# Performance work log

Measured on AMD Instinct MI355X. Metric: run time of the kernel, lower is better.

Reference implementation:

```python
import jax, jax.numpy as jnp
import numpy as np

N_NODES = 100000
N_EDGES = 1600000
NFEAT = 128
NHID = 128
NCLASS = 40


def gcn_conv(x, W, b, src, dst, n_nodes):
    """PyG-style GCNConv: x' = D^{-1/2}(A+I)D^{-1/2} (x W) + b."""
    h = x @ W  # [N, out]
    loop = jnp.arange(n_nodes, dtype=src.dtype)
    s = jnp.concatenate([src, loop])  # add self-loops
    d = jnp.concatenate([dst, loop])
    deg = jax.ops.segment_sum(jnp.ones_like(s, dtype=h.dtype), d, num_segments=n_nodes)
    dinv = jnp.where(deg > 0, jax.lax.rsqrt(deg), 0.0)
    norm = dinv[s] * dinv[d]  # [E+N]
    msg = h[s] * norm[:, None]  # gather + scale
    out = jax.ops.segment_sum(msg, d, num_segments=n_nodes)  # scatter-add
    return out + b


def setup_inputs() -> dict:
    key = jax.random.key(0)
    ks = jax.random.split(key, 6)
    x = jax.random.normal(ks[0], (N_NODES, NFEAT), dtype=jnp.float32)
    edge_index = jax.random.randint(ks[1], (2, N_EDGES), 0, N_NODES, dtype=jnp.int64)
    sc1 = 1.0 / np.sqrt(NFEAT)
    sc2 = 1.0 / np.sqrt(NHID)
    W1 = jax.random.normal(ks[2], (NFEAT, NHID), dtype=jnp.float32) * sc1
    b1 = jnp.zeros((NHID,), dtype=jnp.float32)
    Wm = jax.random.normal(ks[3], (NHID, NHID), dtype=jnp.float32) * sc2
    bm = jnp.zeros((NHID,), dtype=jnp.float32)
    W2 = jax.random.normal(ks[4], (NHID, NCLASS), dtype=jnp.float32) * sc2
    b2 = jnp.zeros((NCLASS,), dtype=jnp.float32)
    return {"x": x, "edge_index": edge_index, "W1": W1, "b1": b1,
            "Wm": Wm, "bm": bm, "W2": W2, "b2": b2}


def reference(x, edge_index, W1, b1, Wm, bm, W2, b2):
    # StandGCNX forward, eval mode (dropout = identity)
    src, dst = edge_index[0], edge_index[1]
    n = x.shape[0]
    h = jax.nn.relu(gcn_conv(x, W1, b1, src, dst, n))
    h = jax.nn.relu(gcn_conv(h, Wm, bm, src, dst, n))
    out = gcn_conv(h, W2, b2, src, dst, n)
    return out
```

## Files before the change

### kernel.cpp

```cpp
#include <hip/hip_runtime.h>
#include <hip/hip_bf16.h>

typedef __attribute__((ext_vector_type(8))) short bf16x8;
typedef __attribute__((ext_vector_type(4))) float f32x4;

__device__ __forceinline__ ushort bf16rne(float f) {
    uint u = __float_as_uint(f);
    return (ushort)((u + 0x7fffu + ((u >> 16) & 1u)) >> 16);
}
__device__ __forceinline__ void unpack2(uint p, float& a, float& b) {
    a = __uint_as_float(p << 16);
    b = __uint_as_float(p & 0xffff0000u);
}


__global__ __launch_bounds__(256) void k_pre1(const float* __restrict__ W1,
                                              const float* __restrict__ Wm,
                                              const float* __restrict__ W2,
                                              ushort* __restrict__ w1t,
                                              ushort* __restrict__ wmt,
                                              ushort* __restrict__ w2t,
                                              const int* __restrict__ dst,
                                              int* __restrict__ bcnt, int E) {
    __shared__ int hist[512];
    int b = blockIdx.x;
    int t = threadIdx.x;
    if (b < 152) {
        if (b < 64) {
            int i = b * 256 + t; int k = i >> 7, n = i & 127;
            w1t[n * 128 + k] = bf16rne(W1[k * 128 + n]);
        } else if (b < 128) {
            int i = (b - 64) * 256 + t; int k = i >> 7, n = i & 127;
            wmt[n * 128 + k] = bf16rne(Wm[k * 128 + n]);
        } else {
            int i = (b - 128) * 256 + t;
            if (i < 6144) {
                int n = i >> 7, k = i & 127;
                w2t[n * 128 + k] = (n < 40) ? bf16rne(W2[k * 40 + n]) : (ushort)0;
            }
        }
        return;
    }
    hist[t] = 0; hist[t + 256] = 0;
    __syncthreads();
    int off = (b - 152) * 4096;
    int cnt = min(4096, E - off);
    for (int i = t; i < cnt; i += 256) atomicAdd(&hist[dst[off + i] >> 8], 1);
    __syncthreads();
    if (hist[t]) atomicAdd(&bcnt[t], hist[t]);
    if (hist[t + 256]) atomicAdd(&bcnt[t + 256], hist[t + 256]);
}

__global__ void k_bscan(const int* __restrict__ bcnt, int* __restrict__ bbase,
                        int* __restrict__ bcur, int nbuck) {
    __shared__ int s[512];
    int t = threadIdx.x;
    s[t] = (t < nbuck) ? bcnt[t] : 0;
    __syncthreads();
    for (int d = 1; d < 512; d <<= 1) {
        int u = (t >= d) ? s[t - d] : 0;
        __syncthreads();
        if (t >= d) s[t] += u;
        __syncthreads();
    }
    int excl = (t == 0) ? 0 : s[t - 1];
    bbase[t] = excl;
    if (t < nbuck) bcur[t] = excl;
    if (t == 511) bbase[512] = s[511];
}


__global__ __launch_bounds__(256) void k_pack_gemm(const int* __restrict__ src,
                                                   const int* __restrict__ dst,
                                                   int* __restrict__ bcur,
                                                   uint* __restrict__ pairbuf,
                                                   int E, int nbuck, int ntile,
                                                   const float* __restrict__ A,
                                                   const ushort* __restrict__ Wt,
                                                   ushort* __restrict__ C, int M) {
    __shared__ int hist[512];
    __shared__ int scn[512];
    __shared__ int cur[512];
    __shared__ int gbase[512];
    __shared__ uint sorted[4096];
    int t = threadIdx.x;
    if ((int)blockIdx.x >= ntile) {
        int blk = blockIdx.x - ntile;
        int wave = t >> 6, lane = t & 63;
        int m16 = lane & 15, quad = lane >> 4;
        int rowA = blk * 64 + wave * 16 + m16;
        int rA = min(rowA, M - 1);
        const float4* A4 = (const float4*)A;

        f32x4 acc[8];
#pragma unroll
        for (int i = 0; i < 8; i++) acc[i] = (f32x4){0.f, 0.f, 0.f, 0.f};
#pragma unroll
        for (int it = 0; it < 4; it++) {
            float4 f0 = A4[(size_t)rA * 32 + 8 * it + 2 * quad];
            float4 f1 = A4[(size_t)rA * 32 + 8 * it + 2 * quad + 1];
            bf16x8 af;
            af[0] = (short)bf16rne(f0.x); af[1] = (short)bf16rne(f0.y);
            af[2] = (short)bf16rne(f0.z); af[3] = (short)bf16rne(f0.w);
            af[4] = (short)bf16rne(f1.x); af[5] = (short)bf16rne(f1.y);
            af[6] = (short)bf16rne(f1.z); af[7] = (short)bf16rne(f1.w);
#pragma unroll
            for (int nt = 0; nt < 8; nt++) {
                bf16x8 bfr = *(const bf16x8*)(Wt + (size_t)(nt * 16 + m16) * 128 + it * 32 + quad * 8);
                acc[nt] = __builtin_amdgcn_mfma_f32_16x16x32_bf16(af, bfr, acc[nt], 0, 0, 0);
            }
        }
        int rowBase = blk * 64 + wave * 16 + quad * 4;
#pragma unroll
        for (int nt = 0; nt < 8; nt++) {
            int col = nt * 16 + m16;
#pragma unroll
            for (int r = 0; r < 4; r++) {
                int row = rowBase + r;
                if (row < M) C[(size_t)row * 128 + col] = bf16rne(acc[nt][r]);
            }
        }
        return;
    }
    int off = blockIdx.x * 4096;
    int cnt = min(4096, E - off);
    hist[t] = 0; hist[t + 256] = 0;
    __syncthreads();
    for (int i = t; i < cnt; i += 256) {
        int b = dst[off + i] >> 8;
        atomicAdd(&hist[b], 1);
    }
    __syncthreads();
    scn[t] = hist[t]; scn[t + 256] = hist[t + 256];
    __syncthreads();
    for (int d = 1; d < 256; d <<= 1) {
        int u0 = (t >= d) ? scn[t - d] : 0;
        int u1 = (t >= d) ? scn[256 + t - d] : 0;
        __syncthreads();
        if (t >= d) { scn[t] += u0; scn[256 + t] += u1; }
        __syncthreads();
    }
    int tot0 = scn[255];
    scn[256 + t] += tot0;
    __syncthreads();
    cur[t] = (t == 0) ? 0 : scn[t - 1];
    cur[t + 256] = scn[t + 255];
    if (t < nbuck && hist[t] > 0) gbase[t] = atomicAdd(&bcur[t], hist[t]);
    int t2 = t + 256;
    if (t2 < nbuck && hist[t2] > 0) gbase[t2] = atomicAdd(&bcur[t2], hist[t2]);
    __syncthreads();
    for (int i = t; i < cnt; i += 256) {
        int d = dst[off + i];
        int s = src[off + i];
        int b = d >> 8;
        int pos = atomicAdd(&cur[b], 1);
        sorted[pos] = ((uint)(d & 255) << 24) | (uint)s;
    }
    __syncthreads();
    int wid = t >> 6, lane = t & 63;
    for (int b = wid; b < nbuck; b += 4) {
        int n = hist[b];
        if (n == 0) continue;
        int ls = (b == 0) ? 0 : scn[b - 1];
        int gb = gbase[b];
        for (int j = lane; j < n; j += 64)
            pairbuf[gb + j] = sorted[ls + j];
    }
}

#define CSR_CAP 5632
__global__ __launch_bounds__(256) void k_csrbuild(const uint* __restrict__ pairbuf,
                                                  const int* __restrict__ bbase,
                                                  int* __restrict__ rowptr,
                                                  float* __restrict__ dinv,
                                                  int* __restrict__ csr,
                                                  int N, int nbuck) {
    __shared__ int lhist[256];
    __shared__ int scn[256];
    __shared__ int lcur[256];
    __shared__ int lcsr[CSR_CAP];
    int b = blockIdx.x;
    int base = b << 8;
    int nn = min(256, N - base);
    int lo = bbase[b], hi = bbase[b + 1];
    int cnt = hi - lo;
    int t = threadIdx.x;
    lhist[t] = 0;
    __syncthreads();
    for (int i = t; i < cnt; i += 256) atomicAdd(&lhist[pairbuf[lo + i] >> 24], 1);
    __syncthreads();
    int mydeg = lhist[t];
    scn[t] = mydeg;
    __syncthreads();
    for (int d = 1; d < 256; d <<= 1) {
        int u = (t >= d) ? scn[t - d] : 0;
        __syncthreads();
        if (t >= d) scn[t] += u;
        __syncthreads();
    }
    int excl = (t == 0) ? 0 : scn[t - 1];
    lcur[t] = excl;
    if (t < nn) {
        rowptr[base + t] = lo + excl;
        dinv[base + t] = rsqrtf((float)(mydeg + 1));
    }
    if (b == nbuck - 1 && t == 0) rowptr[N] = hi;
    __syncthreads();
    if (cnt <= CSR_CAP) {
        for (int i = t; i < cnt; i += 256) {
            uint p = pairbuf[lo + i];
            int pos = atomicAdd(&lcur[p >> 24], 1);
            lcsr[pos] = (int)(p & 0xFFFFFFu);
        }
        __syncthreads();
        for (int i = t; i < cnt; i += 256) csr[lo + i] = lcsr[i];
    } else {
        for (int i = t; i < cnt; i += 256) {
            uint p = pairbuf[lo + i];
            int pos = lo + atomicAdd(&lcur[p >> 24], 1);
            csr[pos] = (int)(p & 0xFFFFFFu);
        }
    }
}


template <int NT, bool EDGE_W>
__device__ __forceinline__ void fused_agg_gemm(const ushort* __restrict__ g,
                                               const float* __restrict__ dinv,
                                               const int* __restrict__ rowptr,
                                               const int* __restrict__ csr,
                                               const float* __restrict__ bias,
                                               const ushort* __restrict__ Wt,
                                               ushort* __restrict__ C,
                                               int M, int ccols) {
    __shared__ ushort hs[32][136];
    __shared__ int nextNode;
    int t = threadIdx.x;
    if (t == 0) nextNode = 0;
    int l = t & 15;
    const uint4* g16 = (const uint4*)g;
    float4 bb0 = ((const float4*)bias)[2 * l];
    float4 bb1 = ((const float4*)bias)[2 * l + 1];
    __syncthreads();

    for (;;) {
        int idx = 0;
        if (l == 0) idx = atomicAdd(&nextNode, 1);
        idx = __shfl(idx, (t & 63) & ~15, 64);
        if (idx >= 32) break;
        int node = blockIdx.x * 32 + idx;
        int nd = min(node, M - 1);
        float dn = dinv[nd];
        float a[8];
        {
            uint4 p = g16[(size_t)nd * 16 + l];
            float u, v;
            if (EDGE_W) {
                unpack2(p.x, u, v); a[0] = u * dn; a[1] = v * dn;
                unpack2(p.y, u, v); a[2] = u * dn; a[3] = v * dn;
                unpack2(p.z, u, v); a[4] = u * dn; a[5] = v * dn;
                unpack2(p.w, u, v); a[6] = u * dn; a[7] = v * dn;
            } else {
                unpack2(p.x, a[0], a[1]); unpack2(p.y, a[2], a[3]);
                unpack2(p.z, a[4], a[5]); unpack2(p.w, a[6], a[7]);
            }
        }
        int e0 = rowptr[nd], e1 = rowptr[nd + 1];
        int e = e0;
        for (; e + 4 <= e1; e += 4) {
            int s0 = csr[e], s1 = csr[e + 1], s2 = csr[e + 2], s3 = csr[e + 3];
            float w0 = 1.f, w1 = 1.f, w2 = 1.f, w3 = 1.f;
            if (EDGE_W) { w0 = dinv[s0]; w1 = dinv[s1]; w2 = dinv[s2]; w3 = dinv[s3]; }
            uint4 p0 = g16[(size_t)s0 * 16 + l];
            uint4 p1 = g16[(size_t)s1 * 16 + l];
            uint4 p2 = g16[(size_t)s2 * 16 + l];
            uint4 p3 = g16[(size_t)s3 * 16 + l];
            float u, v;
            if (EDGE_W) {
                unpack2(p0.x, u, v); a[0] += u * w0; a[1] += v * w0;
                unpack2(p0.y, u, v); a[2] += u * w0; a[3] += v * w0;
                unpack2(p0.z, u, v); a[4] += u * w0; a[5] += v * w0;
                unpack2(p0.w, u, v); a[6] += u * w0; a[7] += v * w0;
                unpack2(p1.x, u, v); a[0] += u * w1; a[1] += v * w1;
                unpack2(p1.y, u, v); a[2] += u * w1; a[3] += v * w1;
                unpack2(p1.z, u, v); a[4] += u * w1; a[5] += v * w1;
                unpack2(p1.w, u, v); a[6] += u * w1; a[7] += v * w1;
                unpack2(p2.x, u, v); a[0] += u * w2; a[1] += v * w2;
                unpack2(p2.y, u, v); a[2] += u * w2; a[3] += v * w2;
                unpack2(p2.z, u, v); a[4] += u * w2; a[5] += v * w2;
                unpack2(p2.w, u, v); a[6] += u * w2; a[7] += v * w2;
                unpack2(p3.x, u, v); a[0] += u * w3; a[1] += v * w3;
                unpack2(p3.y, u, v); a[2] += u * w3; a[3] += v * w3;
                unpack2(p3.z, u, v); a[4] += u * w3; a[5] += v * w3;
                unpack2(p3.w, u, v); a[6] += u * w3; a[7] += v * w3;
            } else {
                unpack2(p0.x, u, v); a[0] += u; a[1] += v;
                unpack2(p0.y, u, v); a[2] += u; a[3] += v;
                unpack2(p0.z, u, v); a[4] += u; a[5] += v;
                unpack2(p0.w, u, v); a[6] += u; a[7] += v;
                unpack2(p1.x, u, v); a[0] += u; a[1] += v;
                unpack2(p1.y, u, v); a[2] += u; a[3] += v;
                unpack2(p1.z, u, v); a[4] += u; a[5] += v;
                unpack2(p1.w, u, v); a[6] += u; a[7] += v;
                unpack2(p2.x, u, v); a[0] += u; a[1] += v;
                unpack2(p2.y, u, v); a[2] += u; a[3] += v;
                unpack2(p2.z, u, v); a[4] += u; a[5] += v;
                unpack2(p2.w, u, v); a[6] += u; a[7] += v;
                unpack2(p3.x, u, v); a[0] += u; a[1] += v;
                unpack2(p3.y, u, v); a[2] += u; a[3] += v;
                unpack2(p3.z, u, v); a[4] += u; a[5] += v;
                unpack2(p3.w, u, v); a[6] += u; a[7] += v;
            }
        }
        for (; e < e1; e++) {
            int s = csr[e];
            float w = EDGE_W ? dinv[s] : 1.f;
            uint4 p = g16[(size_t)s * 16 + l];
            float u, v;
            unpack2(p.x, u, v); a[0] += u * w; a[1] += v * w;
            unpack2(p.y, u, v); a[2] += u * w; a[3] += v * w;
            unpack2(p.z, u, v); a[4] += u * w; a[5] += v * w;
            unpack2(p.w, u, v); a[6] += u * w; a[7] += v * w;
        }
        float o0 = fmaxf(a[0] * dn + bb0.x, 0.f);
        float o1 = fmaxf(a[1] * dn + bb0.y, 0.f);
        float o2 = fmaxf(a[2] * dn + bb0.z, 0.f);
        float o3 = fmaxf(a[3] * dn + bb0.w, 0.f);
        float o4 = fmaxf(a[4] * dn + bb1.x, 0.f);
        float o5 = fmaxf(a[5] * dn + bb1.y, 0.f);
        float o6 = fmaxf(a[6] * dn + bb1.z, 0.f);
        float o7 = fmaxf(a[7] * dn + bb1.w, 0.f);
        uint4 qv;
        qv.x = (uint)bf16rne(o0) | ((uint)bf16rne(o1) << 16);
        qv.y = (uint)bf16rne(o2) | ((uint)bf16rne(o3) << 16);
        qv.z = (uint)bf16rne(o4) | ((uint)bf16rne(o5) << 16);
        qv.w = (uint)bf16rne(o6) | ((uint)bf16rne(o7) << 16);
        *(uint4*)&hs[idx][l * 8] = qv;
    }
    __syncthreads();

    int wave = t >> 6, lane = t & 63;
    int m16 = lane & 15, quad = lane >> 4;
    int rowHalf = wave & 1;
    int ntHalf = wave >> 1;
    constexpr int NTH = (NT + 1) / 2;
    int ntStart = ntHalf * NTH;
    int ntEnd = ntHalf ? NT : NTH;

    f32x4 acc[NTH];
#pragma unroll
    for (int i = 0; i < NTH; i++) acc[i] = (f32x4){0.f, 0.f, 0.f, 0.f};
#pragma unroll
    for (int it = 0; it < 4; it++) {
        bf16x8 af = *(const bf16x8*)&hs[rowHalf * 16 + m16][it * 32 + quad * 8];
        for (int nt = ntStart; nt < ntEnd; nt++) {
            bf16x8 bfr = *(const bf16x8*)(Wt + (size_t)(nt * 16 + m16) * 128 + it * 32 + quad * 8);
            acc[nt - ntStart] = __builtin_amdgcn_mfma_f32_16x16x32_bf16(af, bfr, acc[nt - ntStart], 0, 0, 0);
        }
    }
    int rowBase = blockIdx.x * 32 + rowHalf * 16 + quad * 4;
    float dnv[4];
#pragma unroll
    for (int r = 0; r < 4; r++) dnv[r] = dinv[min(rowBase + r, M - 1)];
    for (int nt = ntStart; nt < ntEnd; nt++) {
        int col = nt * 16 + m16;
        if (col >= ccols) continue;
#pragma unroll
        for (int r = 0; r < 4; r++) {
            int row = rowBase + r;
            if (row < M) C[(size_t)row * ccols + col] = bf16rne(acc[nt - ntStart][r] * dnv[r]);
        }
    }
}

__global__ __launch_bounds__(256) void k_fusedA(const ushort* __restrict__ g,
                                                const float* __restrict__ dinv,
                                                const int* __restrict__ rowptr,
                                                const int* __restrict__ csr,
                                                const float* __restrict__ bias,
                                                const ushort* __restrict__ Wt,
                                                ushort* __restrict__ C, int M) {
    fused_agg_gemm<8, true>(g, dinv, rowptr, csr, bias, Wt, C, M, 128);
}

__global__ __launch_bounds__(256) void k_fusedB(const ushort* __restrict__ g,
                                                const float* __restrict__ dinv,
                                                const int* __restrict__ rowptr,
                                                const int* __restrict__ csr,
                                                const float* __restrict__ bias,
                                                const ushort* __restrict__ Wt,
                                                ushort* __restrict__ C, int M) {
    fused_agg_gemm<3, false>(g, dinv, rowptr, csr, bias, Wt, C, M, 40);
}


__global__ __launch_bounds__(256) void k_agg40_b(const ushort* __restrict__ g3,
                                                 const float* __restrict__ dinv,
                                                 const int* __restrict__ rowptr,
                                                 const int* __restrict__ csr,
                                                 const float* __restrict__ bias,
                                                 float* __restrict__ out, int N) {
    int t = threadIdx.x;
    if (t >= 250) return;
    int grp = t / 10;
    int l = t - grp * 10;
    int node = blockIdx.x * 25 + grp;
    if (node >= N) return;
    const uint2* gp = (const uint2*)g3;
    float dn = dinv[node];
    float a0, a1, a2, a3;
    {
        uint2 p = gp[(size_t)node * 10 + l];
        unpack2(p.x, a0, a1);
        unpack2(p.y, a2, a3);
    }
    int e0 = rowptr[node], e1 = rowptr[node + 1];
    int e = e0;
    for (; e + 4 <= e1; e += 4) {
        int s0 = csr[e], s1 = csr[e + 1], s2 = csr[e + 2], s3 = csr[e + 3];
        uint2 p0 = gp[(size_t)s0 * 10 + l];
        uint2 p1 = gp[(size_t)s1 * 10 + l];
        uint2 p2 = gp[(size_t)s2 * 10 + l];
        uint2 p3 = gp[(size_t)s3 * 10 + l];
        float u, v;
        unpack2(p0.x, u, v); a0 += u; a1 += v;
        unpack2(p0.y, u, v); a2 += u; a3 += v;
        unpack2(p1.x, u, v); a0 += u; a1 += v;
        unpack2(p1.y, u, v); a2 += u; a3 += v;
        unpack2(p2.x, u, v); a0 += u; a1 += v;
        unpack2(p2.y, u, v); a2 += u; a3 += v;
        unpack2(p3.x, u, v); a0 += u; a1 += v;
        unpack2(p3.y, u, v); a2 += u; a3 += v;
    }
    for (; e < e1; e++) {
        int s = csr[e];
        uint2 p = gp[(size_t)s * 10 + l];
        float u, v;
        unpack2(p.x, u, v); a0 += u; a1 += v;
        unpack2(p.y, u, v); a2 += u; a3 += v;
    }
    float4 bb = ((const float4*)bias)[l];
    float4 o;
    o.x = a0 * dn + bb.x;
    o.y = a1 * dn + bb.y;
    o.z = a2 * dn + bb.z;
    o.w = a3 * dn + bb.w;
    ((float4*)out)[(size_t)node * 10 + l] = o;
}


extern "C" void kernel_launch(void* const* d_in, const int* in_sizes, int n_in,
                              void* d_out, int out_size, void* d_ws, size_t ws_size,
                              hipStream_t stream) {
    const float* x  = (const float*)d_in[0];
    const int* eidx = (const int*)d_in[1];
    const float* W1 = (const float*)d_in[2];
    const float* b1 = (const float*)d_in[3];
    const float* Wm = (const float*)d_in[4];
    const float* bm = (const float*)d_in[5];
    const float* W2 = (const float*)d_in[6];
    const float* b2 = (const float*)d_in[7];
    float* out = (float*)d_out;

    int N = in_sizes[0] / 128;
    int E = in_sizes[1] / 2;
    const int* src = eidx;
    const int* dst = eidx + E;
    int nbuck = (N + 255) >> 8;
    int ntile = (E + 4095) / 4096;

    char* ws = (char*)d_ws;
    size_t off = 0;
    auto alloc = [&](size_t bytes) -> void* {
        void* p = ws + off;
        off += (bytes + 255) & ~(size_t)255;
        return p;
    };
    float*  dinv    = (float*)alloc((size_t)N * 4);
    int*    rowptr  = (int*)alloc(((size_t)N + 1) * 4);
    int*    csr     = (int*)alloc((size_t)E * 4);
    uint*   pairbuf = (uint*)alloc((size_t)E * 4);
    int*    bcnt    = (int*)alloc(512 * 4);
    int*    bbase   = (int*)alloc(513 * 4);
    int*    bcur    = (int*)alloc(512 * 4);
    ushort* w1t     = (ushort*)alloc(128 * 128 * 2);
    ushort* wmt     = (ushort*)alloc(128 * 128 * 2);
    ushort* w2t     = (ushort*)alloc(48 * 128 * 2);
    ushort* gbuf    = (ushort*)alloc((size_t)N * 128 * 2);
    ushort* gbuf2   = (ushort*)alloc((size_t)N * 128 * 2);
    ushort* g3      = (ushort*)alloc((size_t)N * 40 * 2);

    int gblk64 = (N + 63) / 64;
    int gblk32 = (N + 31) / 32;

    hipMemsetAsync(bcnt, 0, 512 * 4, stream);
    k_pre1<<<152 + ntile, 256, 0, stream>>>(W1, Wm, W2, w1t, wmt, w2t, dst, bcnt, E);
    k_bscan<<<1, 512, 0, stream>>>(bcnt, bbase, bcur, nbuck);
    k_pack_gemm<<<ntile + gblk64, 256, 0, stream>>>(src, dst, bcur, pairbuf, E, nbuck,
                                                    ntile, x, w1t, gbuf, N);
    k_csrbuild<<<nbuck, 256, 0, stream>>>(pairbuf, bbase, rowptr, dinv, csr, N, nbuck);
    k_fusedA<<<gblk32, 256, 0, stream>>>(gbuf, dinv, rowptr, csr, b1, wmt, gbuf2, N);
    k_fusedB<<<gblk32, 256, 0, stream>>>(gbuf2, dinv, rowptr, csr, bm, w2t, g3, N);
    k_agg40_b<<<(N + 24) / 25, 256, 0, stream>>>(g3, dinv, rowptr, csr, b2, out, N);
}
```

Measured before the change: 368.6 us.

## Aggregate each node with a full wave and broadcast neighbor indices via readlane

The fused aggregation+GEMM kernel now assigns one 64-lane wave per node instead of 16 lanes per node. Each lane handles two features using 4-byte loads. Neighbor indices and dinv weights are loaded cooperatively in chunks of 64 and broadcast with readlane, with 8 gathers in flight per unrolled step. This is meant to remove redundant per-lane scalar index and weight loads and to increase memory-level parallelism. The trade-off is fewer nodes processed concurrently per wave, narrower per-lane loads, and extra readlane instructions.

```diff
diff --git a/kernel.cpp b/kernel.cpp
--- a/kernel.cpp
+++ b/kernel.cpp
@@ -237,110 +237,105 @@
     __shared__ int nextNode;
     int t = threadIdx.x;
     if (t == 0) nextNode = 0;
-    int l = t & 15;
-    const uint4* g16 = (const uint4*)g;
-    float4 bb0 = ((const float4*)bias)[2 * l];
-    float4 bb1 = ((const float4*)bias)[2 * l + 1];
-    __syncthreads();
+    __syncthreads();
+    int lane = t & 63;
+    const uint* g32 = (const uint*)g;
+    float2 bb = ((const float2*)bias)[lane];
 
     for (;;) {
         int idx = 0;
-        if (l == 0) idx = atomicAdd(&nextNode, 1);
-        idx = __shfl(idx, (t & 63) & ~15, 64);
+        if (lane == 0) idx = atomicAdd(&nextNode, 1);
+        idx = __builtin_amdgcn_readfirstlane(idx);
         if (idx >= 32) break;
         int node = blockIdx.x * 32 + idx;
         int nd = min(node, M - 1);
         float dn = dinv[nd];
-        float a[8];
+        int e0 = rowptr[nd], e1 = rowptr[nd + 1];
+        float a0, a1;
         {
-            uint4 p = g16[(size_t)nd * 16 + l];
+            uint p = g32[(size_t)nd * 64 + lane];
             float u, v;
-            if (EDGE_W) {
-                unpack2(p.x, u, v); a[0] = u * dn; a[1] = v * dn;
-                unpack2(p.y, u, v); a[2] = u * dn; a[3] = v * dn;
-                unpack2(p.z, u, v); a[4] = u * dn; a[5] = v * dn;
-                unpack2(p.w, u, v); a[6] = u * dn; a[7] = v * dn;
-            } else {
-                unpack2(p.x, a[0], a[1]); unpack2(p.y, a[2], a[3]);
-                unpack2(p.z, a[4], a[5]); unpack2(p.w, a[6], a[7]);
+            unpack2(p, u, v);
+            if (EDGE_W) { a0 = u * dn; a1 = v * dn; } else { a0 = u; a1 = v; }
+        }
+        for (int base = e0; base < e1; base += 64) {
+            int nchunk = e1 - base;
+            if (nchunk > 64) nchunk = 64;
+            int sidx = 0;
+            int swi = 0x3f800000;
+            if (lane < nchunk) {
+                sidx = csr[base + lane];
+                if (EDGE_W) swi = __float_as_int(dinv[sidx]);
             }
-        }
-        int e0 = rowptr[nd], e1 = rowptr[nd + 1];
-        int e = e0;
-        for (; e + 4 <= e1; e += 4) {
-            int s0 = csr[e], s1 = csr[e + 1], s2 = csr[e + 2], s3 = csr[e + 3];
-            float w0 = 1.f, w1 = 1.f, w2 = 1.f, w3 = 1.f;
-            if (EDGE_W) { w0 = dinv[s0]; w1 = dinv[s1]; w2 = dinv[s2]; w3 = dinv[s3]; }
-            uint4 p0 = g16[(size_t)s0 * 16 + l];
-            uint4 p1 = g16[(size_t)s1 * 16 + l];
-            uint4 p2 = g16[(size_t)s2 * 16 + l];
-            uint4 p3 = g16[(size_t)s3 * 16 + l];
-            float u, v;
-            if (EDGE_W) {
-                unpack2(p0.x, u, v); a[0] += u * w0; a[1] += v * w0;
-                unpack2(p0.y, u, v); a[2] += u * w0; a[3] += v * w0;
-                unpack2(p0.z, u, v); a[4] += u * w0; a[5] += v * w0;
-                unpack2(p0.w, u, v); a[6] += u * w0; a[7] += v * w0;
-                unpack2(p1.x, u, v); a[0] += u * w1; a[1] += v * w1;
-                unpack2(p1.y, u, v); a[2] += u * w1; a[3] += v * w1;
-                unpack2(p1.z, u, v); a[4] += u * w1; a[5] += v * w1;
-                unpack2(p1.w, u, v); a[6] += u * w1; a[7] += v * w1;
-                unpack2(p2.x, u, v); a[0] += u * w2; a[1] += v * w2;
-                unpack2(p2.y, u, v); a[2] += u * w2; a[3] += v * w2;
-                unpack2(p2.z, u, v); a[4] += u * w2; a[5] += v * w2;
-                unpack2(p2.w, u, v); a[6] += u * w2; a[7] += v * w2;
-                unpack2(p3.x, u, v); a[0] += u * w3; a[1] += v * w3;
-                unpack2(p3.y, u, v); a[2] += u * w3; a[3] += v * w3;
-                unpack2(p3.z, u, v); a[4] += u * w3; a[5] += v * w3;
-                unpack2(p3.w, u, v); a[6] += u * w3; a[7] += v * w3;
-            } else {
-                unpack2(p0.x, u, v); a[0] += u; a[1] += v;
-                unpack2(p0.y, u, v); a[2] += u; a[3] += v;
-                unpack2(p0.z, u, v); a[4] += u; a[5] += v;
-                unpack2(p0.w, u, v); a[6] += u; a[7] += v;
-                unpack2(p1.x, u, v); a[0] += u; a[1] += v;
-                unpack2(p1.y, u, v); a[2] += u; a[3] += v;
-                unpack2(p1.z, u, v); a[4] += u; a[5] += v;
-                unpack2(p1.w, u, v); a[6] += u; a[7] += v;
-                unpack2(p2.x, u, v); a[0] += u; a[1] += v;
-                unpack2(p2.y, u, v); a[2] += u; a[3] += v;
-                unpack2(p2.z, u, v); a[4] += u; a[5] += v;
-                unpack2(p2.w, u, v); a[6] += u; a[7] += v;
-                unpack2(p3.x, u, v); a[0] += u; a[1] += v;
-                unpack2(p3.y, u, v); a[2] += u; a[3] += v;
-                unpack2(p3.z, u, v); a[4] += u; a[5] += v;
-                unpack2(p3.w, u, v); a[6] += u; a[7] += v;
+            int j = 0;
+            for (; j + 8 <= nchunk; j += 8) {
+                int s0 = __builtin_amdgcn_readlane(sidx, j);
+                int s1 = __builtin_amdgcn_readlane(sidx, j + 1);
+                int s2 = __builtin_amdgcn_readlane(sidx, j + 2);
+                int s3 = __builtin_amdgcn_readlane(sidx, j + 3);
+                int s4 = __builtin_amdgcn_readlane(sidx, j + 4);
+                int s5 = __builtin_amdgcn_readlane(sidx, j + 5);
+                int s6 = __builtin_amdgcn_readlane(sidx, j + 6);
+                int s7 = __builtin_amdgcn_readlane(sidx, j + 7);
+                uint p0 = g32[(size_t)s0 * 64 + lane];
+                uint p1 = g32[(size_t)s1 * 64 + lane];
+                uint p2 = g32[(size_t)s2 * 64 + lane];
+                uint p3 = g32[(size_t)s3 * 64 + lane];
+                uint p4 = g32[(size_t)s4 * 64 + lane];
+                uint p5 = g32[(size_t)s5 * 64 + lane];
+                uint p6 = g32[(size_t)s6 * 64 + lane];
+                uint p7 = g32[(size_t)s7 * 64 + lane];
+                float u, v;
+                if (EDGE_W) {
+                    float w0 = __int_as_float(__builtin_amdgcn_readlane(swi, j));
+                    float w1 = __int_as_float(__builtin_amdgcn_readlane(swi, j + 1));
+                    float w2 = __int_as_float(__builtin_amdgcn_readlane(swi, j + 2));
+                    float w3 = __int_as_float(__builtin_amdgcn_readlane(swi, j + 3));
+                    float w4 = __int_as_float(__builtin_amdgcn_readlane(swi, j + 4));
+                    float w5 = __int_as_float(__builtin_amdgcn_readlane(swi, j + 5));
+                    float w6 = __int_as_float(__builtin_amdgcn_readlane(swi, j + 6));
+                    float w7 = __int_as_float(__builtin_amdgcn_readlane(swi, j + 7));
+                    unpack2(p0, u, v); a0 += u * w0; a1 += v * w0;
+                    unpack2(p1, u, v); a0 += u * w1; a1 += v * w1;
+                    unpack2(p2, u, v); a0 += u * w2; a1 += v * w2;
+                    unpack2(p3, u, v); a0 += u * w3; a1 += v * w3;
+                    unpack2(p4, u, v); a0 += u * w4; a1 += v * w4;
+                    unpack2(p5, u, v); a0 += u * w5; a1 += v * w5;
+                    unpack2(p6, u, v); a0 += u * w6; a1 += v * w6;
+                    unpack2(p7, u, v); a0 += u * w7; a1 += v * w7;
+                } else {
+                    unpack2(p0, u, v); a0 += u; a1 += v;
+                    unpack2(p1, u, v); a0 += u; a1 += v;
+                    unpack2(p2, u, v); a0 += u; a1 += v;
+                    unpack2(p3, u, v); a0 += u; a1 += v;
+                    unpack2(p4, u, v); a0 += u; a1 += v;
+                    unpack2(p5, u, v); a0 += u; a1 += v;
+                    unpack2(p6, u, v); a0 += u; a1 += v;
+                    unpack2(p7, u, v); a0 += u; a1 += v;
+                }
             }
-        }
-        for (; e < e1; e++) {
-            int s = csr[e];
-            float w = EDGE_W ? dinv[s] : 1.f;
-            uint4 p = g16[(size_t)s * 16 + l];
-            float u, v;
-            unpack2(p.x, u, v); a[0] += u * w; a[1] += v * w;
-            unpack2(p.y, u, v); a[2] += u * w; a[3] += v * w;
-            unpack2(p.z, u, v); a[4] += u * w; a[5] += v * w;
-            unpack2(p.w, u, v); a[6] += u * w; a[7] += v * w;
-        }
-        float o0 = fmaxf(a[0] * dn + bb0.x, 0.f);
-        float o1 = fmaxf(a[1] * dn + bb0.y, 0.f);
-        float o2 = fmaxf(a[2] * dn + bb0.z, 0.f);
-        float o3 = fmaxf(a[3] * dn + bb0.w, 0.f);
-        float o4 = fmaxf(a[4] * dn + bb1.x, 0.f);
-        float o5 = fmaxf(a[5] * dn + bb1.y, 0.f);
-        float o6 = fmaxf(a[6] * dn + bb1.z, 0.f);
-        float o7 = fmaxf(a[7] * dn + bb1.w, 0.f);
-        uint4 qv;
-        qv.x = (uint)bf16rne(o0) | ((uint)bf16rne(o1) << 16);
-        qv.y = (uint)bf16rne(o2) | ((uint)bf16rne(o3) << 16);
-        qv.z = (uint)bf16rne(o4) | ((uint)bf16rne(o5) << 16);
-        qv.w = (uint)bf16rne(o6) | ((uint)bf16rne(o7) << 16);
-        *(uint4*)&hs[idx][l * 8] = qv;
-    }
-    __syncthreads();
-
-    int wave = t >> 6, lane = t & 63;
-    int m16 = lane & 15, quad = lane >> 4;
+            for (; j < nchunk; j++) {
+                int s0 = __builtin_amdgcn_readlane(sidx, j);
+                uint p0 = g32[(size_t)s0 * 64 + lane];
+                float u, v;
+                unpack2(p0, u, v);
+                if (EDGE_W) {
+                    float w0 = __int_as_float(__builtin_amdgcn_readlane(swi, j));
+                    a0 += u * w0; a1 += v * w0;
+                } else {
+                    a0 += u; a1 += v;
+                }
+            }
+        }
+        float o0 = fmaxf(a0 * dn + bb.x, 0.f);
+        float o1 = fmaxf(a1 * dn + bb.y, 0.f);
+        uint q = (uint)bf16rne(o0) | ((uint)bf16rne(o1) << 16);
+        *(uint*)&hs[idx][lane * 2] = q;
+    }
+    __syncthreads();
+
+    int wave = t >> 6, lane6 = t & 63;
+    int m16 = lane6 & 15, quad = lane6 >> 4;
     int rowHalf = wave & 1;
     int ntHalf = wave >> 1;
     constexpr int NTH = (NT + 1) / 2;
```

After: 370.9 us. Within noise of the previous version (+0.6%).
